# Optimization experiments

Measured on AMD Instinct MI355X. Metric: run time of the kernel, lower is better.

The kernel has to match this reference:

```python
import jax, jax.numpy as jnp
import numpy as np

DEPTH_BINS = 39
FEAT = 64
IMG_H, IMG_W = 448, 800
DS = 16
HF, WF = IMG_H // DS, IMG_W // DS  # 28, 50
D_MIN, D_MAX = 2.0, 80.0
BEV_X0 = 0.0
BEV_Y0 = -50.4
RES = 0.8
HB, WB = 188, 126
BN_EPS = 1e-5


def make_frustum():
    # (D, Hf, Wf, 3) points (u*d, v*d, d) at receptive-field centers
    step = (D_MAX - D_MIN) / DEPTH_BINS
    depths = jnp.linspace(D_MIN + step / 2, D_MAX - step / 2, DEPTH_BINS)
    u = jnp.arange(WF, dtype=jnp.float32) * DS + DS / 2
    v = jnp.arange(HF, dtype=jnp.float32) * DS + DS / 2
    d = jnp.broadcast_to(depths[:, None, None], (DEPTH_BINS, HF, WF))
    ug = jnp.broadcast_to(u[None, None, :], (DEPTH_BINS, HF, WF))
    vg = jnp.broadcast_to(v[None, :, None], (DEPTH_BINS, HF, WF))
    return jnp.stack([ug * d, vg * d, d], axis=-1)


def conv2d(x, w, b):
    y = jax.lax.conv_general_dilated(x, w, (1, 1), 'SAME', dimension_numbers=('NCHW', 'OIHW', 'NCHW'))
    return y + b[None, :, None, None]


def bn(x, g, b, m, v):
    s = (g * jax.lax.rsqrt(v + BN_EPS))[None, :, None, None]
    return (x - m[None, :, None, None]) * s + b[None, :, None, None]


def lss_forward(head, intrinsics, car2cams, w1, b1, g1, be1, m1, v1, w2, b2, g2, be2, m2, v2, w3, b3, g3, be3, m3, v3, w4, b4):
    B, N = intrinsics.shape[:2]
    # CamEncoder head: depth softmax x feature outer product (lift)
    depth = jax.nn.softmax(head[:, :DEPTH_BINS], axis=1)       # (BN, D, Hf, Wf)
    feat = head[:, DEPTH_BINS:]                                # (BN, C, Hf, Wf)
    vol = depth[:, :, None] * feat[:, None]                    # (BN, D, C, Hf, Wf)
    vol = vol.reshape(B, N, DEPTH_BINS, FEAT, HF, WF).transpose(0, 1, 2, 4, 5, 3)  # (B,N,D,Hf,Wf,C)
    # get_geometry: frustum -> car frame
    frustum = make_frustum()
    frust_h = jnp.concatenate([frustum, jnp.ones((DEPTH_BINS, HF, WF, 1), jnp.float32)], axis=-1)
    inv_K3 = jnp.linalg.inv(intrinsics)
    inv_K = jnp.zeros((B, N, 4, 4), jnp.float32).at[..., :3, :3].set(inv_K3).at[..., 3, 3].set(1.0)
    T = jnp.linalg.inv(car2cams) @ inv_K                       # (B,N,4,4)
    geom = jnp.einsum('bnij,dhwj->bndhwi', T, frust_h)[..., :3]  # (B,N,D,Hf,Wf,3)
    # voxel_pool: masked scatter-add into BEV grid (int cast truncates toward 0, matching torch .long())
    bx = ((geom[..., 0] - BEV_X0) / RES).astype(jnp.int32)
    by = ((geom[..., 1] - BEV_Y0) / RES).astype(jnp.int32)
    mask = (bx >= 0) & (bx < HB) & (by >= 0) & (by < WB)
    M = N * DEPTH_BINS * HF * WF
    feat_flat = (vol * mask[..., None]).reshape(B * M, FEAT)
    idx = jnp.where(mask, bx * WB + by, 0).reshape(B, M)
    idx = (idx + jnp.arange(B)[:, None] * (HB * WB)).reshape(-1)
    bev = jax.ops.segment_sum(feat_flat, idx, num_segments=B * HB * WB)
    bev = bev.reshape(B, HB, WB, FEAT).transpose(0, 3, 1, 2)   # (B,C,HB,WB)
    # BEVDecoder (eval-mode BN)
    x = jax.nn.relu(bn(conv2d(bev, w1, b1), g1, be1, m1, v1))
    x = jax.nn.relu(bn(conv2d(x, w2, b2), g2, be2, m2, v2))
    x = jax.nn.relu(bn(conv2d(x, w3, b3), g3, be3, m3, v3))
    return conv2d(x, w4, b4)                                   # (B,1,HB,WB)


def setup_inputs() -> dict:
    key = jax.random.key(0)
    ks = jax.random.split(key, 8)
    B, N = 2, 6
    head = jax.random.normal(ks[0], (B * N, DEPTH_BINS + FEAT, HF, WF), dtype=jnp.float32)
    # realistic invertible intrinsics
    f = 500.0 + 25.0 * jax.random.normal(ks[1], (B, N))
    K = (jnp.zeros((B, N, 3, 3))
         .at[..., 0, 0].set(f).at[..., 1, 1].set(f)
         .at[..., 0, 2].set(IMG_W / 2).at[..., 1, 2].set(IMG_H / 2)
         .at[..., 2, 2].set(1.0)).astype(jnp.float32)
    # cam->car rotation: car X = cam z (forward), car Y = -cam x, car Z = -cam y (up)
    R = jnp.array([[0.0, 0.0, 1.0], [-1.0, 0.0, 0.0], [0.0, -1.0, 0.0]], jnp.float32)
    t = jnp.array([2.0, 0.0, 1.3], jnp.float32) + 0.3 * jax.random.normal(ks[2], (B, N, 3))
    cam2car = (jnp.zeros((B, N, 4, 4))
               .at[..., :3, :3].set(R).at[..., :3, 3].set(t).at[..., 3, 3].set(1.0))
    car2cams = jnp.linalg.inv(cam2car).astype(jnp.float32)

    def w(k, shape, fan_in):
        return jax.random.normal(k, shape, dtype=jnp.float32) * (1.0 / np.sqrt(fan_in))

    inp = dict(head=head, intrinsics=K, car2cams=car2cams)
    inp.update(w1=w(ks[3], (128, FEAT, 3, 3), FEAT * 9), b1=jnp.zeros(128), g1=jnp.ones(128), be1=jnp.zeros(128), m1=jnp.zeros(128), v1=jnp.ones(128))
    inp.update(w2=w(ks[4], (128, 128, 3, 3), 128 * 9), b2=jnp.zeros(128), g2=jnp.ones(128), be2=jnp.zeros(128), m2=jnp.zeros(128), v2=jnp.ones(128))
    inp.update(w3=w(ks[5], (64, 128, 3, 3), 128 * 9), b3=jnp.zeros(64), g3=jnp.ones(64), be3=jnp.zeros(64), m3=jnp.zeros(64), v3=jnp.ones(64))
    inp.update(w4=w(ks[6], (1, 64, 1, 1), 64), b4=jnp.zeros(1))
    return inp


def reference(head, intrinsics, car2cams, w1, b1, g1, be1, m1, v1, w2, b2, g2, be2, m2, v2, w3, b3, g3, be3, m3, v3, w4, b4):
    return lss_forward(head, intrinsics, car2cams, w1, b1, g1, be1, m1, v1, w2, b2, g2, be2, m2, v2, w3, b3, g3, be3, m3, v3, w4, b4)
```

## Files before the change

### kernel.cpp

```cpp
#include <hip/hip_runtime.h>
#include <hip/hip_bf16.h>
#include <math.h>

#define NDEPTH 39
#define NFEAT 64
#define HF 28
#define WF 50
#define NPIXCAM (HF*WF)
#define HB 188
#define WB 126
#define NB (HB*WB)
#define BATCH 2
#define NCAM 12
#define NPIX (BATCH*NB)
#define NCELL NPIX
#define CH_IN (NDEPTH+NFEAT)
#define NPT (NCAM*NPIXCAM)
#define NPD (NPT*NDEPTH)
#define CPAD 16
#define SCAN_NB ((NCELL + 255) / 256)

typedef short bf16x8 __attribute__((ext_vector_type(8)));
typedef float f32x4 __attribute__((ext_vector_type(4)));

#define OFF_DIAG 0u
#define OFF_T    64u
#define OFF_B1   1024u
#define OFF_B2   1536u
#define OFF_B3   2048u
#define OFF_WP1  4096u
#define OFF_WP2  151552u
#define OFF_WP3  446464u
#define OFF_XIN  593920u
#define OFF_X1   6658048u
#define OFF_X2   18786304u
#define OFF_PROBS 30914560u
#define OFF_FEATT 33535360u
#define OFF_CUR   35685760u
#define OFF_START 38717824u
#define OFF_BSUM  38907392u
#define OFF_REC   38908416u
#define WS_NEEDED 44150016u

__device__ inline float bfraw2f(unsigned short u) {
  union { unsigned int i; float f; } c; c.i = ((unsigned int)u) << 16; return c.f;
}
__device__ inline float ldf(const void* p, size_t i, int mode) {
  if (mode == 0) return ((const float*)p)[i];
  if (mode == 1) return bfraw2f(((const unsigned short*)p)[i]);
  return (float)(((const _Float16*)p)[i]);
}

__global__ __launch_bounds__(256) void canary_kernel(float* out, int n, float val) {
  int i = blockIdx.x * 256 + threadIdx.x;
  if (i < n) out[i] = val;
}
__global__ __launch_bounds__(256) void probe_kernel(float* out, int n) {
  int i = blockIdx.x * 256 + threadIdx.x;
  if (i < n) out[i] = 16.0f;
}
__global__ void detect_mode_kernel(const void* g1, int* diag) {
  if (threadIdx.x == 0) {
    unsigned int bits = *(const unsigned int*)g1;
    int m = -1;
    if (bits == 0x3F800000u) m = 0;
    else if (bits == 0x3F803F80u) m = 1;
    else if (bits == 0x3C003C00u) m = 2;
    diag[0] = m;
  }
}

__global__ __launch_bounds__(64) void compute_T_kernel(
    const void* __restrict__ K, const void* __restrict__ C,
    const int* __restrict__ diag, float* __restrict__ T) {
  int i = threadIdx.x;
  if (i >= NCAM) return;
  int md = diag[0];
  if (md < 0) return;
  double a = ldf(K, i*9+0, md), b = ldf(K, i*9+1, md), c = ldf(K, i*9+2, md),
         d = ldf(K, i*9+3, md), e = ldf(K, i*9+4, md), f = ldf(K, i*9+5, md),
         g = ldf(K, i*9+6, md), h = ldf(K, i*9+7, md), ii = ldf(K, i*9+8, md);
  double det = a * (e * ii - f * h) - b * (d * ii - f * g) + c * (d * h - e * g);
  double id = 1.0 / det;
  double iK[4][4] = {
      {(e * ii - f * h) * id, (c * h - b * ii) * id, (b * f - c * e) * id, 0.0},
      {(f * g - d * ii) * id, (a * ii - c * g) * id, (c * d - a * f) * id, 0.0},
      {(d * h - e * g) * id, (b * g - a * h) * id, (a * e - b * d) * id, 0.0},
      {0.0, 0.0, 0.0, 1.0}};
  double M[4][8];
  for (int r = 0; r < 4; ++r)
    for (int cc = 0; cc < 4; ++cc) {
      M[r][cc] = ldf(C, (size_t)i * 16 + r * 4 + cc, md);
      M[r][cc + 4] = (r == cc) ? 1.0 : 0.0;
    }
  for (int col = 0; col < 4; ++col) {
    int piv = col;
    double pv = fabs(M[col][col]);
    for (int r = col + 1; r < 4; ++r) {
      double v = fabs(M[r][col]);
      if (v > pv) { pv = v; piv = r; }
    }
    if (piv != col)
      for (int cc = 0; cc < 8; ++cc) {
        double t = M[col][cc]; M[col][cc] = M[piv][cc]; M[piv][cc] = t;
      }
    double inv = 1.0 / M[col][col];
    for (int cc = 0; cc < 8; ++cc) M[col][cc] *= inv;
    for (int r = 0; r < 4; ++r)
      if (r != col) {
        double fa = M[r][col];
        for (int cc = 0; cc < 8; ++cc) M[r][cc] -= fa * M[col][cc];
      }
  }
  for (int r = 0; r < 4; ++r)
    for (int cc = 0; cc < 4; ++cc) {
      double sv = 0.0;
      for (int j = 0; j < 4; ++j) sv += M[r][4 + j] * iK[j][cc];
      T[i * 16 + r * 4 + cc] = (float)sv;
    }
}

__global__ void check_T_kernel(const float* __restrict__ T, int* diag) {
  if (threadIdx.x != 0 || blockIdx.x != 0) return;
  int bad = 0;
  for (int i = 0; i < NCAM * 16; ++i) {
    float x = T[i];
    if (!isfinite(x) || fabsf(x) > 1e7f) bad = 1;
  }
  for (int c = 0; c < NCAM; ++c)
    if (fabsf(T[c * 16 + 15] - 1.0f) > 0.01f) bad = 1;
  if (bad) diag[1] = 1;
}

template <int CIN, int COUT>
__global__ __launch_bounds__(256) void pack_kernel(
    const void* __restrict__ w, const void* __restrict__ bconv,
    const void* __restrict__ g, const void* __restrict__ be,
    const void* __restrict__ m, const void* __restrict__ v,
    const int* __restrict__ diag, __hip_bfloat16* __restrict__ wp,
    float* __restrict__ bias) {
  int md = diag[0];
  if (md < 0) return;
  int t = blockIdx.x * 256 + threadIdx.x;
  if (t < COUT) {
    float s = ldf(g, t, md) * (1.0f / sqrtf(ldf(v, t, md) + 1e-5f));
    bias[t] = (ldf(bconv, t, md) - ldf(m, t, md)) * s + ldf(be, t, md);
  }
  if (t >= 9 * CIN * COUT) return;
  constexpr int NOCB = COUT / 16, NICB = CIN / 32;
  int j = t & 7;
  int l = (t >> 3) & 63;
  int tile = t >> 9;
  int ocb = tile % NOCB;
  int rest = tile / NOCB;
  int icb = rest % NICB;
  int kykx = rest / NICB;
  int ic = icb * 32 + (l >> 4) * 8 + j;
  int oc = ocb * 16 + (l & 15);
  int ky = kykx / 3, kx = kykx - ky * 3;
  float s = ldf(g, oc, md) * (1.0f / sqrtf(ldf(v, oc, md) + 1e-5f));
  float wv = ldf(w, ((size_t)(oc * CIN + ic) * 3 + ky) * 3 + kx, md) * s;
  wp[t] = __float2bfloat16(wv);
}

__device__ inline int point_cell(const float* __restrict__ T, int cam, int rem, int d) {
  int h = rem / WF;
  int w = rem - h * WF;
  const float* Tm = T + cam * 16;
  float u = w * 16.0f + 8.0f;
  float v = h * 16.0f + 8.0f;
  float dep = 3.0f + 2.0f * d;
  float ud = u * dep, vd = v * dep;
  float gx = Tm[0] * ud + Tm[1] * vd + Tm[2] * dep + Tm[3];
  float gy = Tm[4] * ud + Tm[5] * vd + Tm[6] * dep + Tm[7];
  int bx = (int)((gx - 0.0f) / 0.8f);
  int by = (int)((gy - (-50.4f)) / 0.8f);
  if (bx >= 0 && bx < HB && by >= 0 && by < WB) {
    int b = cam / 6;
    return b * NB + bx * WB + by;
  }
  return -1;
}

__global__ __launch_bounds__(64) void prep_kernel2(
    const void* __restrict__ head, const float* __restrict__ T,
    const int* __restrict__ diag, float* __restrict__ probs,
    __hip_bfloat16* __restrict__ featT, int* __restrict__ curpad) {
  int md = diag[0];
  if (md < 0) return;
  int pix = blockIdx.x;
  int cam = pix / NPIXCAM;
  int rem = pix - cam * NPIXCAM;
  int lane = threadIdx.x;
  size_t base = (size_t)cam * CH_IN * NPIXCAM;

  float logit = (lane < NDEPTH) ? ldf(head, base + (size_t)lane * NPIXCAM + rem, md)
                                : -INFINITY;
  float mx = logit;
  for (int o = 32; o; o >>= 1) mx = fmaxf(mx, __shfl_xor(mx, o, 64));
  float e = (lane < NDEPTH) ? expf(logit - mx) : 0.0f;
  float s = e;
  for (int o = 32; o; o >>= 1) s += __shfl_xor(s, o, 64);
  if (lane < NDEPTH) probs[(size_t)pix * NDEPTH + lane] = e / s;

  float feat = ldf(head, base + (size_t)(NDEPTH + lane) * NPIXCAM + rem, md);
  featT[(size_t)pix * NFEAT + lane] = __float2bfloat16(feat);

  if (lane < NDEPTH) {
    int cell = point_cell(T, cam, rem, lane);
    if (cell >= 0) atomicAdd(&curpad[cell * CPAD], 1);
  }
}

__global__ __launch_bounds__(256) void scan_phase1(
    const int* __restrict__ curpad, int* __restrict__ start,
    int* __restrict__ bsum) {
  int cell = blockIdx.x * 256 + threadIdx.x;
  int c = (cell < NCELL) ? curpad[cell * CPAD] : 0;
  __shared__ int sh[256];
  sh[threadIdx.x] = c;
  __syncthreads();
  for (int off = 1; off < 256; off <<= 1) {
    int t = (threadIdx.x >= off) ? sh[threadIdx.x - off] : 0;
    __syncthreads();
    sh[threadIdx.x] += t;
    __syncthreads();
  }
  if (cell < NCELL) start[cell] = sh[threadIdx.x] - c;
  if (threadIdx.x == 255) bsum[blockIdx.x] = sh[255];
}

__global__ __launch_bounds__(256) void scan_phase2(
    int* __restrict__ bsum, int* __restrict__ start) {
  int tid = threadIdx.x;
  int v = (tid < SCAN_NB) ? bsum[tid] : 0;
  __shared__ int sh[256];
  sh[tid] = v;
  __syncthreads();
  for (int off = 1; off < 256; off <<= 1) {
    int t = (tid >= off) ? sh[tid - off] : 0;
    __syncthreads();
    sh[tid] += t;
    __syncthreads();
  }
  if (tid < SCAN_NB) bsum[tid] = sh[tid] - v;
  if (tid == SCAN_NB - 1) start[NCELL] = sh[tid];
}

__global__ __launch_bounds__(256) void scan_phase3(
    int* __restrict__ curpad, int* __restrict__ start,
    const int* __restrict__ bsum) {
  int cell = blockIdx.x * 256 + threadIdx.x;
  if (cell >= NCELL) return;
  int v = start[cell] + bsum[blockIdx.x];
  start[cell] = v;
  curpad[cell * CPAD] = v;
}

__global__ __launch_bounds__(256) void fill_kernel(
    const float* __restrict__ probs, const float* __restrict__ T,
    const int* __restrict__ diag, int* __restrict__ curpad,
    unsigned long long* __restrict__ rec) {
  int md = diag[0];
  if (md < 0) return;
  int tid = blockIdx.x * 256 + threadIdx.x;
  if (tid >= NPD) return;
  int d = tid / NPT;
  int pix = tid - d * NPT;
  int cam = pix / NPIXCAM;
  int rem = pix - cam * NPIXCAM;
  int cell = point_cell(T, cam, rem, d);
  if (cell < 0) return;
  float p = probs[(size_t)pix * NDEPTH + d];
  int pos = atomicAdd(&curpad[cell * CPAD], 1);
  rec[pos] = ((unsigned long long)__float_as_uint(p) << 32) | (unsigned)pix;
}

__global__ __launch_bounds__(256) void gather_kernel(
    const unsigned long long* __restrict__ rec, const int* __restrict__ start,
    const __hip_bfloat16* __restrict__ featT, __hip_bfloat16* __restrict__ xin) {
  int cell = blockIdx.x;
  int wv = threadIdx.x >> 6;
  int lane = threadIdx.x & 63;
  int s0 = start[cell], s1 = start[cell + 1];
  const unsigned short* ft = (const unsigned short*)featT;
  float acc = 0.0f;
  int j = s0 + wv;
  for (; j + 12 < s1; j += 16) {
    unsigned long long r0 = rec[j];
    unsigned long long r1 = rec[j + 4];
    unsigned long long r2 = rec[j + 8];
    unsigned long long r3 = rec[j + 12];
    float f0 = bfraw2f(ft[(size_t)(unsigned)(r0 & 0xFFFFFFFFull) * NFEAT + lane]);
    float f1 = bfraw2f(ft[(size_t)(unsigned)(r1 & 0xFFFFFFFFull) * NFEAT + lane]);
    float f2 = bfraw2f(ft[(size_t)(unsigned)(r2 & 0xFFFFFFFFull) * NFEAT + lane]);
    float f3 = bfraw2f(ft[(size_t)(unsigned)(r3 & 0xFFFFFFFFull) * NFEAT + lane]);
    acc += __uint_as_float((unsigned)(r0 >> 32)) * f0;
    acc += __uint_as_float((unsigned)(r1 >> 32)) * f1;
    acc += __uint_as_float((unsigned)(r2 >> 32)) * f2;
    acc += __uint_as_float((unsigned)(r3 >> 32)) * f3;
  }
  for (; j < s1; j += 4) {
    unsigned long long r = rec[j];
    acc += __uint_as_float((unsigned)(r >> 32)) *
           bfraw2f(ft[(size_t)(unsigned)(r & 0xFFFFFFFFull) * NFEAT + lane]);
  }
  __shared__ float red[4][64];
  red[wv][lane] = acc;
  __syncthreads();
  if (threadIdx.x < 64) {
    float tot = red[0][lane] + red[1][lane] + red[2][lane] + red[3][lane];
    xin[(size_t)cell * NFEAT + lane] = __float2bfloat16(tot);
  }
}

template <int CIN, int COUT>
__global__ __launch_bounds__(256) void conv_mfma_kernel(
    const __hip_bfloat16* __restrict__ in, const __hip_bfloat16* __restrict__ wp,
    const float* __restrict__ bias, __hip_bfloat16* __restrict__ out) {
  constexpr int NICB = CIN / 32, NOCB = COUT / 16;
  int wv = threadIdx.x >> 6;
  int l = threadIdx.x & 63;
  int pw = blockIdx.x * 64 + wv * 16;
  if (pw >= NPIX) return;
  int m = l & 15;
  int jg = l >> 4;
  int p = pw + m;
  int bq = p / NB;
  int rr = p - bq * NB;
  int y = rr / WB;
  int x = rr - y * WB;

  f32x4 acc[NOCB] = {};

  for (int kykx = 0; kykx < 9; ++kykx) {
    int ky = kykx / 3;
    int dy = ky - 1, dx = kykx - ky * 3 - 1;
    int yy = y + dy, xx = x + dx;
    bool valid = (yy >= 0) & (yy < HB) & (xx >= 0) & (xx < WB);
    int yyc = valid ? yy : 0, xxc = valid ? xx : 0;
    const __hip_bfloat16* arow =
        in + ((size_t)(bq * HB + yyc) * WB + xxc) * CIN + jg * 8;
    const __hip_bfloat16* wpk = wp + (size_t)(kykx * NICB * NOCB) * 512 + l * 8;
#pragma unroll
    for (int icb = 0; icb < NICB; ++icb) {
      bf16x8 a = valid ? *reinterpret_cast<const bf16x8*>(arow + icb * 32)
                       : (bf16x8)(short)0;
#pragma unroll
      for (int ocb = 0; ocb < NOCB; ++ocb) {
        bf16x8 b = *reinterpret_cast<const bf16x8*>(wpk + (icb * NOCB + ocb) * 512);
        acc[ocb] = __builtin_amdgcn_mfma_f32_16x16x32_bf16(a, b, acc[ocb], 0, 0, 0);
      }
    }
  }
#pragma unroll
  for (int ocb = 0; ocb < NOCB; ++ocb) {
    int oc = ocb * 16 + m;
    float bv = bias[oc];
#pragma unroll
    for (int r = 0; r < 4; ++r) {
      int pix = pw + jg * 4 + r;
      float vo = fmaxf(acc[ocb][r] + bv, 0.0f);
      out[(size_t)pix * COUT + oc] = __float2bfloat16(vo);
    }
  }
}

__global__ __launch_bounds__(256) void conv1x1_kernel(
    const __hip_bfloat16* __restrict__ in, const void* __restrict__ w4,
    const void* __restrict__ b4, const int* __restrict__ diag,
    float* __restrict__ out, int npix) {
  int md = diag[0];
  if (md < 0) return;
  int p = blockIdx.x * 256 + threadIdx.x;
  if (p >= npix) return;
  const unsigned short* ip = (const unsigned short*)(in + (size_t)p * NFEAT);
  float acc = 0.0f;
#pragma unroll
  for (int i = 0; i < NFEAT; ++i) acc += bfraw2f(ip[i]) * ldf(w4, i, md);
  out[p] = acc + ldf(b4, 0, md);
}

__global__ __launch_bounds__(256) void final_check_kernel(
    const int* __restrict__ diag, const int* __restrict__ start,
    float* out, int n) {
  float v = 0.0f;
  if (diag[0] < 0) v = 300.0f;
  else if (diag[1]) v = 200.0f;
  else if (start[NCELL] == 0) v = 100.0f;
  if (v == 0.0f) return;
  int i = blockIdx.x * 256 + threadIdx.x;
  if (i < n) out[i] = v;
}

static inline int cdiv(long long a, long long b) { return (int)((a + b - 1) / b); }

extern "C" void kernel_launch(void* const* d_in, const int* in_sizes, int n_in,
                              void* d_out, int out_size, void* d_ws, size_t ws_size,
                              hipStream_t stream) {
  float* out = (float*)d_out;
  size_t out_bytes = (size_t)out_size * sizeof(float);

  hipStreamCaptureStatus cst = hipStreamCaptureStatusNone;
  (void)hipStreamIsCapturing(stream, &cst);
  const bool capturing = (cst != hipStreamCaptureStatusNone);
  hipStream_t s = capturing ? stream : (hipStream_t)0;

#define FINISH()                                                      \
  do {                                                                \
    if (!capturing) {                                                 \
      (void)hipStreamSynchronize(s);                                  \
      (void)hipStreamSynchronize(stream);                             \
      (void)hipDeviceSynchronize();                                   \
    }                                                                 \
  } while (0)

  (void)hipMemsetAsync(d_out, 0x40, out_bytes, s);
  probe_kernel<<<cdiv(out_size, 256), 256, 0, s>>>(out, out_size);

  if (n_in != 23 || in_sizes[0] != NCAM * CH_IN * NPIXCAM) {
    canary_kernel<<<cdiv(out_size, 256), 256, 0, s>>>(out, out_size, 500.0f + n_in);
    FINISH(); return;
  }
  if (in_sizes[1] != NCAM * 9 || in_sizes[2] != NCAM * 16 ||
      in_sizes[3] != 128 * 64 * 9) {
    canary_kernel<<<cdiv(out_size, 256), 256, 0, s>>>(out, out_size, 610.0f);
    FINISH(); return;
  }
  if (out_size != NPIX) {
    canary_kernel<<<cdiv(out_size, 256), 256, 0, s>>>(out, out_size, 700.0f);
    FINISH(); return;
  }
  if (ws_size < WS_NEEDED) {
    canary_kernel<<<cdiv(out_size, 256), 256, 0, s>>>(
        out, out_size, 1000.0f + (float)(ws_size >> 20));
    FINISH(); return;
  }

  const void* head = d_in[0];
  const void* intr = d_in[1];
  const void* c2c  = d_in[2];

  char* ws = (char*)d_ws;
  int*   diag = (int*)(ws + OFF_DIAG);
  float* T    = (float*)(ws + OFF_T);
  float* bb1 = (float*)(ws + OFF_B1);
  float* bb2 = (float*)(ws + OFF_B2);
  float* bb3 = (float*)(ws + OFF_B3);
  __hip_bfloat16* wp1 = (__hip_bfloat16*)(ws + OFF_WP1);
  __hip_bfloat16* wp2 = (__hip_bfloat16*)(ws + OFF_WP2);
  __hip_bfloat16* wp3 = (__hip_bfloat16*)(ws + OFF_WP3);
  __hip_bfloat16* xin = (__hip_bfloat16*)(ws + OFF_XIN);
  __hip_bfloat16* x1  = (__hip_bfloat16*)(ws + OFF_X1);
  __hip_bfloat16* x2  = (__hip_bfloat16*)(ws + OFF_X2);
  __hip_bfloat16* x3  = (__hip_bfloat16*)(ws + OFF_XIN);
  float* probs = (float*)(ws + OFF_PROBS);
  __hip_bfloat16* featT = (__hip_bfloat16*)(ws + OFF_FEATT);
  int* curpad = (int*)(ws + OFF_CUR);
  int* start  = (int*)(ws + OFF_START);
  int* bsum   = (int*)(ws + OFF_BSUM);
  unsigned long long* rec = (unsigned long long*)(ws + OFF_REC);

  (void)hipMemsetAsync(diag, 0, 16, s);
  detect_mode_kernel<<<1, 64, 0, s>>>(d_in[5], diag);
  compute_T_kernel<<<1, 64, 0, s>>>(intr, c2c, diag, T);
  check_T_kernel<<<1, 64, 0, s>>>(T, diag);
  pack_kernel<64, 128><<<288, 256, 0, s>>>(d_in[3], d_in[4], d_in[5], d_in[6],
                                           d_in[7], d_in[8], diag, wp1, bb1);
  pack_kernel<128, 128><<<576, 256, 0, s>>>(d_in[9], d_in[10], d_in[11], d_in[12],
                                            d_in[13], d_in[14], diag, wp2, bb2);
  pack_kernel<128, 64><<<288, 256, 0, s>>>(d_in[15], d_in[16], d_in[17], d_in[18],
                                           d_in[19], d_in[20], diag, wp3, bb3);

  (void)hipMemsetAsync(curpad, 0, (size_t)NCELL * CPAD * 4, s);
  prep_kernel2<<<NPT, 64, 0, s>>>(head, T, diag, probs, featT, curpad);
  scan_phase1<<<SCAN_NB, 256, 0, s>>>(curpad, start, bsum);
  scan_phase2<<<1, 256, 0, s>>>(bsum, start);
  scan_phase3<<<SCAN_NB, 256, 0, s>>>(curpad, start, bsum);
  fill_kernel<<<cdiv(NPD, 256), 256, 0, s>>>(probs, T, diag, curpad, rec);
  gather_kernel<<<NCELL, 256, 0, s>>>(rec, start, featT, xin);

  conv_mfma_kernel<64, 128><<<cdiv(NPIX, 64), 256, 0, s>>>(xin, wp1, bb1, x1);
  conv_mfma_kernel<128, 128><<<cdiv(NPIX, 64), 256, 0, s>>>(x1, wp2, bb2, x2);
  conv_mfma_kernel<128, 64><<<cdiv(NPIX, 64), 256, 0, s>>>(x2, wp3, bb3, x3);
  conv1x1_kernel<<<cdiv(NPIX, 256), 256, 0, s>>>(x3, d_in[21], d_in[22], diag,
                                                 out, NPIX);
  final_check_kernel<<<cdiv(NPIX, 256), 256, 0, s>>>(diag, start, out, NPIX);
  FINISH();
#undef FINISH
}
```

Before: 300.4 us.

## Tile prep kernel through shared memory and split histogram into separate kernel

Replaces the one-block-per-pixel prep kernel, whose head reads are strided across channels, with a kernel that loads a 64-pixel tile of all channels into shared memory. Each thread then computes the depth softmax for its own pixel, and the tile is written out transposed as bf16 features. The per-point cell histogram with atomics moves into its own kernel with one thread per (depth, pixel) point, ordered depth-major. This cuts the block count and makes the global loads coalesced, at the cost of one extra kernel launch and less parallel softmax work per pixel.

```diff
diff --git a/kernel.cpp b/kernel.cpp
--- a/kernel.cpp
+++ b/kernel.cpp
@@ -19,6 +19,8 @@
 #define NPD (NPT*NDEPTH)
 #define CPAD 16
 #define SCAN_NB ((NCELL + 255) / 256)
+#define TPIX 64
+#define TILES_PER_CAM ((NPIXCAM + TPIX - 1) / TPIX)
 
 typedef short bf16x8 __attribute__((ext_vector_type(8)));
 typedef float f32x4 __attribute__((ext_vector_type(4)));
@@ -182,34 +184,57 @@
   return -1;
 }
 
-__global__ __launch_bounds__(64) void prep_kernel2(
-    const void* __restrict__ head, const float* __restrict__ T,
-    const int* __restrict__ diag, float* __restrict__ probs,
-    __hip_bfloat16* __restrict__ featT, int* __restrict__ curpad) {
+__global__ __launch_bounds__(64) void prep_kernel3(
+    const void* __restrict__ head, const int* __restrict__ diag,
+    float* __restrict__ probs, __hip_bfloat16* __restrict__ featT) {
   int md = diag[0];
   if (md < 0) return;
-  int pix = blockIdx.x;
+  int cam = blockIdx.x / TILES_PER_CAM;
+  int t0 = (blockIdx.x - cam * TILES_PER_CAM) * TPIX;
+  int npx = NPIXCAM - t0;
+  if (npx > TPIX) npx = TPIX;
+  int tid = threadIdx.x;
+
+  __shared__ float tile[CH_IN][TPIX + 1];
+  size_t base = (size_t)cam * CH_IN * NPIXCAM + t0;
+  for (int ch = 0; ch < CH_IN; ++ch) {
+    if (tid < npx) tile[ch][tid] = ldf(head, base + (size_t)ch * NPIXCAM + tid, md);
+  }
+  __syncthreads();
+
+  if (tid < npx) {
+    int pix = cam * NPIXCAM + t0 + tid;
+    float mx = -INFINITY;
+#pragma unroll
+    for (int d = 0; d < NDEPTH; ++d) mx = fmaxf(mx, tile[d][tid]);
+    float ssum = 0.0f;
+#pragma unroll
+    for (int d = 0; d < NDEPTH; ++d) ssum += expf(tile[d][tid] - mx);
+#pragma unroll
+    for (int d = 0; d < NDEPTH; ++d)
+      probs[(size_t)pix * NDEPTH + d] = expf(tile[d][tid] - mx) / ssum;
+  }
+  __syncthreads();
+
+  for (int px = 0; px < npx; ++px) {
+    int pix = cam * NPIXCAM + t0 + px;
+    featT[(size_t)pix * NFEAT + tid] = __float2bfloat16(tile[NDEPTH + tid][px]);
+  }
+}
+
+__global__ __launch_bounds__(256) void hist_kernel(
+    const float* __restrict__ T, const int* __restrict__ diag,
+    int* __restrict__ curpad) {
+  int md = diag[0];
+  if (md < 0) return;
+  int tid = blockIdx.x * 256 + threadIdx.x;
+  if (tid >= NPD) return;
+  int d = tid / NPT;
+  int pix = tid - d * NPT;
   int cam = pix / NPIXCAM;
   int rem = pix - cam * NPIXCAM;
-  int lane = threadIdx.x;
-  size_t base = (size_t)cam * CH_IN * NPIXCAM;
-
-  float logit = (lane < NDEPTH) ? ldf(head, base + (size_t)lane * NPIXCAM + rem, md)
-                                : -INFINITY;
-  float mx = logit;
-  for (int o = 32; o; o >>= 1) mx = fmaxf(mx, __shfl_xor(mx, o, 64));
-  float e = (lane < NDEPTH) ? expf(logit - mx) : 0.0f;
-  float s = e;
-  for (int o = 32; o; o >>= 1) s += __shfl_xor(s, o, 64);
-  if (lane < NDEPTH) probs[(size_t)pix * NDEPTH + lane] = e / s;
-
-  float feat = ldf(head, base + (size_t)(NDEPTH + lane) * NPIXCAM + rem, md);
-  featT[(size_t)pix * NFEAT + lane] = __float2bfloat16(feat);
-
-  if (lane < NDEPTH) {
-    int cell = point_cell(T, cam, rem, lane);
-    if (cell >= 0) atomicAdd(&curpad[cell * CPAD], 1);
-  }
+  int cell = point_cell(T, cam, rem, d);
+  if (cell >= 0) atomicAdd(&curpad[cell * CPAD], 1);
 }
 
 __global__ __launch_bounds__(256) void scan_phase1(
@@ -473,7 +498,8 @@
                                            d_in[19], d_in[20], diag, wp3, bb3);
 
   (void)hipMemsetAsync(curpad, 0, (size_t)NCELL * CPAD * 4, s);
-  prep_kernel2<<<NPT, 64, 0, s>>>(head, T, diag, probs, featT, curpad);
+  prep_kernel3<<<NCAM * TILES_PER_CAM, 64, 0, s>>>(head, diag, probs, featT);
+  hist_kernel<<<cdiv(NPD, 256), 256, 0, s>>>(T, diag, curpad);
   scan_phase1<<<SCAN_NB, 256, 0, s>>>(curpad, start, bsum);
   scan_phase2<<<1, 256, 0, s>>>(bsum, start);
   scan_phase3<<<SCAN_NB, 256, 0, s>>>(curpad, start, bsum);
```

New measurement: 326.8 us. +8.8%, slower.
